# Kernel optimization log

Measured on AMD Instinct MI355X. Metric: run time of the kernel, lower is better.

Reference implementation:

```python
import jax, jax.numpy as jnp
import numpy as np

B, D, NB, H = 4096, 1024, 16, 2048
LN_EPS = 1e-5


def setup_inputs() -> dict:
    key = jax.random.key(0)
    ks = jax.random.split(key, 10)
    basis_dim = D * NB
    x = jax.random.normal(ks[0], (B, D), dtype=jnp.float32)
    ln_g = jnp.ones((D,), jnp.float32)
    ln_b = jnp.zeros((D,), jnp.float32)
    centers = jnp.tile(jnp.linspace(-2.0, 2.0, NB, dtype=jnp.float32)[None, :], (D, 1))  # [D, NB]
    width = jnp.ones((D,), jnp.float32)
    fc1_w = jax.random.normal(ks[1], (H, basis_dim), jnp.float32) / np.sqrt(basis_dim)
    fc1_b = jnp.zeros((H,), jnp.float32)
    hm_w = jax.random.normal(ks[2], (1, H), jnp.float32) / np.sqrt(H)
    hm_b = jnp.zeros((1,), jnp.float32)
    hv_w = jax.random.normal(ks[3], (1, H), jnp.float32) / np.sqrt(H)
    hv_b = jnp.zeros((1,), jnp.float32)
    sh_w = jax.random.normal(ks[4], (1, D), jnp.float32) / np.sqrt(D)
    sh_b = jnp.zeros((1,), jnp.float32)
    gamma = jnp.asarray(0.3, jnp.float32)
    return {"x": x, "ln_g": ln_g, "ln_b": ln_b, "centers": centers, "width": width,
            "fc1_w": fc1_w, "fc1_b": fc1_b, "hm_w": hm_w, "hm_b": hm_b,
            "hv_w": hv_w, "hv_b": hv_b, "sh_w": sh_w, "sh_b": sh_b, "gamma": gamma}


def reference(x, ln_g, ln_b, centers, width, fc1_w, fc1_b, hm_w, hm_b, hv_w, hv_b, sh_w, sh_b, gamma):
    # LayerNorm over in_dim
    mu = jnp.mean(x, axis=-1, keepdims=True)
    var = jnp.mean(jnp.square(x - mu), axis=-1, keepdims=True)
    x_n = (x - mu) * jax.lax.rsqrt(var + LN_EPS) * ln_g + ln_b  # [B, D]
    # triangular basis: phi[b,d,k] = relu(1 - |(x_n[b,d] - c[d,k]) / w[d]|)
    w = jax.nn.softplus(width) + 1e-6                              # [D]
    phi = jax.nn.relu(1.0 - jnp.abs((x_n[:, :, None] - centers[None]) / w[None, :, None]))
    z = phi.reshape(x.shape[0], -1)                                # [B, D*NB]
    h = jax.nn.gelu(z @ fc1_w.T + fc1_b, approximate=False)        # [B, H] (dropout = eval identity)
    y_kan_mean = h @ hm_w.T + hm_b                                 # [B, 1]
    y_lin_mean = x_n @ sh_w.T + sh_b                               # [B, 1]
    mean = y_kan_mean + jax.nn.relu(gamma) * y_lin_mean
    log_var = h @ hv_w.T + hv_b
    return (mean, log_var)
```

## Files before the change

kernel.cpp:

```cpp
#include <hip/hip_runtime.h>
#include <hip/hip_bf16.h>

#define BB 4096
#define DD 1024
#define NBF 16
#define HH 2048
#define KK 16384
#define LN_EPS 1e-5f

typedef int   i32x4 __attribute__((ext_vector_type(4)));
typedef float f32x4 __attribute__((ext_vector_type(4)));

__device__ __forceinline__ float softplusf(float x) {
  return (x > 20.f) ? x : log1pf(expf(x));
}
__device__ __forceinline__ int pack4(int q0, int q1, int q2, int q3) {
  return (q0 & 0xff) | ((q1 & 0xff) << 8) | ((q2 & 0xff) << 16) | ((q3 & 0xff) << 24);
}

__global__ void prep_kernel(const float* __restrict__ centers, const float* __restrict__ width,
                            float* __restrict__ cs) {
  const int i = blockIdx.x * 256 + threadIdx.x;
  const int d = i >> 4;
  const float w = softplusf(width[d]) + 1e-6f;
  cs[i] = centers[i] / w;
}

__global__ __launch_bounds__(256)
void zexp_kernel(const float* __restrict__ x, const float* __restrict__ g,
                 const float* __restrict__ be, const float* __restrict__ width,
                 const float* __restrict__ sh_w, const float* __restrict__ sh_b,
                 const float* __restrict__ cs,
                 unsigned char* __restrict__ zq, float* __restrict__ ylin) {
  __shared__ float red[8];
  const int b = blockIdx.x, tid = threadIdx.x;
  const float4 v = ((const float4*)(x + (size_t)b * DD))[tid];
  float s  = v.x + v.y + v.z + v.w;
  float ss = v.x*v.x + v.y*v.y + v.z*v.z + v.w*v.w;
  #pragma unroll
  for (int off = 32; off > 0; off >>= 1) {
    s  += __shfl_xor(s, off);
    ss += __shfl_xor(ss, off);
  }
  if ((tid & 63) == 0) { red[(tid>>6)*2] = s; red[(tid>>6)*2+1] = ss; }
  __syncthreads();
  const float sum   = red[0]+red[2]+red[4]+red[6];
  const float sumsq = red[1]+red[3]+red[5]+red[7];
  const float mu   = sum * (1.f/DD);
  const float var  = sumsq * (1.f/DD) - mu*mu;
  const float rstd = rsqrtf(var + LN_EPS);
  const float4 g4 = ((const float4*)g)[tid];
  const float4 b4 = ((const float4*)be)[tid];
  const float4 w4 = ((const float4*)width)[tid];
  const float4 s4 = ((const float4*)sh_w)[tid];
  const float xn0 = (v.x - mu)*rstd*g4.x + b4.x;
  const float xn1 = (v.y - mu)*rstd*g4.y + b4.y;
  const float xn2 = (v.z - mu)*rstd*g4.z + b4.z;
  const float xn3 = (v.w - mu)*rstd*g4.w + b4.w;
  float xsv[4];
  xsv[0] = xn0 / (softplusf(w4.x) + 1e-6f);
  xsv[1] = xn1 / (softplusf(w4.y) + 1e-6f);
  xsv[2] = xn2 / (softplusf(w4.z) + 1e-6f);
  xsv[3] = xn3 / (softplusf(w4.w) + 1e-6f);
  unsigned char* zr = zq + (size_t)b * KK + tid * 64;
  #pragma unroll
  for (int j = 0; j < 4; ++j) {
    const float4* c4 = (const float4*)(cs + (tid * 4 + j) * 16);
    const float xv = xsv[j];
    int q[16];
    #pragma unroll
    for (int qq = 0; qq < 4; ++qq) {
      const float4 ca = c4[qq];
      q[qq*4+0] = __float2int_rn(fmaxf(0.f, 1.f - fabsf(xv - ca.x)) * 127.f);
      q[qq*4+1] = __float2int_rn(fmaxf(0.f, 1.f - fabsf(xv - ca.y)) * 127.f);
      q[qq*4+2] = __float2int_rn(fmaxf(0.f, 1.f - fabsf(xv - ca.z)) * 127.f);
      q[qq*4+3] = __float2int_rn(fmaxf(0.f, 1.f - fabsf(xv - ca.w)) * 127.f);
    }
    int4 o;
    o.x = pack4(q[0],  q[1],  q[2],  q[3]);
    o.y = pack4(q[4],  q[5],  q[6],  q[7]);
    o.z = pack4(q[8],  q[9],  q[10], q[11]);
    o.w = pack4(q[12], q[13], q[14], q[15]);
    ((int4*)zr)[j] = o;
  }
  float yd = xn0*s4.x + xn1*s4.y + xn2*s4.z + xn3*s4.w;
  #pragma unroll
  for (int off = 32; off > 0; off >>= 1) yd += __shfl_xor(yd, off);
  __syncthreads();
  if ((tid & 63) == 0) red[tid>>6] = yd;
  __syncthreads();
  if (tid == 0) ylin[b] = red[0]+red[1]+red[2]+red[3] + sh_b[0];
}

__global__ __launch_bounds__(256)
void cvt_kernel(const float* __restrict__ w, unsigned char* __restrict__ wq,
                float* __restrict__ wscale) {
  __shared__ float red[4];
  const int j = blockIdx.x, tid = threadIdx.x;
  const float4* row4 = (const float4*)(w + (size_t)j * KK);
  float4 vv[16];
  float mx = 0.f;
  #pragma unroll
  for (int i = 0; i < 16; ++i) {
    vv[i] = row4[tid + i * 256];
    mx = fmaxf(mx, fmaxf(fmaxf(fabsf(vv[i].x), fabsf(vv[i].y)),
                         fmaxf(fabsf(vv[i].z), fabsf(vv[i].w))));
  }
  #pragma unroll
  for (int off = 32; off > 0; off >>= 1) mx = fmaxf(mx, __shfl_xor(mx, off));
  if ((tid & 63) == 0) red[tid >> 6] = mx;
  __syncthreads();
  const float smax = fmaxf(fmaxf(red[0], red[1]), fmaxf(red[2], red[3]));
  const float inv  = (smax > 0.f) ? 127.f / smax : 0.f;
  if (tid == 0) wscale[j] = smax * (1.f / 127.f);
  int* orow = (int*)(wq + (size_t)j * KK);
  #pragma unroll
  for (int i = 0; i < 16; ++i) {
    const int q0 = __float2int_rn(vv[i].x * inv);
    const int q1 = __float2int_rn(vv[i].y * inv);
    const int q2 = __float2int_rn(vv[i].z * inv);
    const int q3 = __float2int_rn(vv[i].w * inv);
    orow[tid + i * 256] = pack4(q0, q1, q2, q3);
  }
}

__global__ __launch_bounds__(256, 2)
void gemm_kernel(const unsigned char* __restrict__ zq, const unsigned char* __restrict__ wq,
                 const float* __restrict__ wscale, const float* __restrict__ fc1_b,
                 float* __restrict__ h) {
  __shared__ unsigned char As[128 * 128];
  __shared__ unsigned char Bs[128 * 128];
  const int tid  = threadIdx.x;
  const int lane = tid & 63;
  const int wv   = tid >> 6;
  const int bid = (blockIdx.x & 7) * 64 + (blockIdx.x >> 3);
  const int bm = bid & 31;
  const int bn = bid >> 5;
  const int wr = wv >> 1, wc = wv & 1;

  i32x4 acc[4][4];
  #pragma unroll
  for (int m = 0; m < 4; ++m)
    #pragma unroll
    for (int n = 0; n < 4; ++n)
      acc[m][n] = (i32x4){0, 0, 0, 0};

  const int srow   = lane >> 3;
  const int schunk = (lane & 7) ^ srow;
  const int frow = lane & 15;
  const int fkb  = lane >> 4;

  const unsigned char* zb  = zq + (size_t)(bm * 128) * KK;
  const unsigned char* wbb = wq + (size_t)(bn * 128) * KK;

  for (int t = 0; t < KK / 128; ++t) {
    const int k0 = t * 128;
    __syncthreads();
    #pragma unroll
    for (int i = 0; i < 4; ++i) {
      const int r = i * 32 + wv * 8 + srow;
      __builtin_amdgcn_global_load_lds(
          (const __attribute__((address_space(1))) void*)(zb + (size_t)r * KK + k0 + schunk * 16),
          (__attribute__((address_space(3))) void*)(&As[(i * 32 + wv * 8) * 128]), 16, 0, 0);
      __builtin_amdgcn_global_load_lds(
          (const __attribute__((address_space(1))) void*)(wbb + (size_t)r * KK + k0 + schunk * 16),
          (__attribute__((address_space(3))) void*)(&Bs[(i * 32 + wv * 8) * 128]), 16, 0, 0);
    }
    __syncthreads();
    #pragma unroll
    for (int ks = 0; ks < 2; ++ks) {
      const int kb = ks * 4 + fkb;
      i32x4 af[4], bfr[4];
      #pragma unroll
      for (int m = 0; m < 4; ++m) {
        const int Ra = wr * 64 + m * 16 + frow;
        af[m] = *reinterpret_cast<const i32x4*>(&As[Ra * 128 + ((kb ^ (Ra & 7)) * 16)]);
      }
      #pragma unroll
      for (int n = 0; n < 4; ++n) {
        const int Rb = wc * 64 + n * 16 + frow;
        bfr[n] = *reinterpret_cast<const i32x4*>(&Bs[Rb * 128 + ((kb ^ (Rb & 7)) * 16)]);
      }
      #pragma unroll
      for (int m = 0; m < 4; ++m)
        #pragma unroll
        for (int n = 0; n < 4; ++n)
          acc[m][n] = __builtin_amdgcn_mfma_i32_16x16x64_i8(af[m], bfr[n], acc[m][n], 0, 0, 0);
    }
  }
  const int row0 = bm * 128 + wr * 64;
  const int col0 = bn * 128 + wc * 64;
  #pragma unroll
  for (int n = 0; n < 4; ++n) {
    const int col = col0 + n * 16 + frow;
    const float sc   = wscale[col] * (1.f / 127.f);
    const float bias = fc1_b[col];
    #pragma unroll
    for (int m = 0; m < 4; ++m) {
      #pragma unroll
      for (int r = 0; r < 4; ++r) {
        const int row = row0 + m * 16 + fkb * 4 + r;
        const float xg = (float)acc[m][n][r] * sc + bias;
        h[(size_t)row * HH + col] = 0.5f * xg * (1.f + erff(xg * 0.70710678118f));
      }
    }
  }
}

__global__ __launch_bounds__(256)
void head_kernel(const float* __restrict__ h, const float* __restrict__ hm_w,
                 const float* __restrict__ hm_b, const float* __restrict__ hv_w,
                 const float* __restrict__ hv_b, const float* __restrict__ ylin,
                 const float* __restrict__ gamma, float* __restrict__ out) {
  __shared__ float red[8];
  const int b = blockIdx.x, tid = threadIdx.x;
  const float4* hr  = (const float4*)(h + (size_t)b * HH);
  const float4* wm  = (const float4*)hm_w;
  const float4* wvv = (const float4*)hv_w;
  float dm = 0.f, dv = 0.f;
  #pragma unroll
  for (int i = 0; i < 2; ++i) {
    const int c = tid + i * 256;
    const float4 hv4 = hr[c];
    const float4 m4  = wm[c];
    const float4 v4  = wvv[c];
    dm += hv4.x*m4.x + hv4.y*m4.y + hv4.z*m4.z + hv4.w*m4.w;
    dv += hv4.x*v4.x + hv4.y*v4.y + hv4.z*v4.z + hv4.w*v4.w;
  }
  #pragma unroll
  for (int off = 32; off > 0; off >>= 1) {
    dm += __shfl_xor(dm, off);
    dv += __shfl_xor(dv, off);
  }
  if ((tid & 63) == 0) { red[(tid>>6)*2] = dm; red[(tid>>6)*2+1] = dv; }
  __syncthreads();
  if (tid == 0) {
    const float sm = red[0]+red[2]+red[4]+red[6] + hm_b[0];
    const float sv = red[1]+red[3]+red[5]+red[7] + hv_b[0];
    out[b]      = sm + fmaxf(gamma[0], 0.f) * ylin[b];
    out[BB + b] = sv;
  }
}

extern "C" void kernel_launch(void* const* d_in, const int* in_sizes, int n_in,
                              void* d_out, int out_size, void* d_ws, size_t ws_size,
                              hipStream_t stream) {
  const float* x       = (const float*)d_in[0];
  const float* ln_g    = (const float*)d_in[1];
  const float* ln_b    = (const float*)d_in[2];
  const float* centers = (const float*)d_in[3];
  const float* width   = (const float*)d_in[4];
  const float* fc1_w   = (const float*)d_in[5];
  const float* fc1_b   = (const float*)d_in[6];
  const float* hm_w    = (const float*)d_in[7];
  const float* hm_b    = (const float*)d_in[8];
  const float* hv_w    = (const float*)d_in[9];
  const float* hv_b    = (const float*)d_in[10];
  const float* sh_w    = (const float*)d_in[11];
  const float* sh_b    = (const float*)d_in[12];
  const float* gamma   = (const float*)d_in[13];

  char* ws = (char*)d_ws;
  float* cs            = (float*)(ws);
  float* ylin          = (float*)(ws + (64 << 10));
  float* wscale        = (float*)(ws + (80 << 10));
  unsigned char* zq    = (unsigned char*)(ws + (1ull << 20));
  unsigned char* wq    = (unsigned char*)(ws + (65ull << 20));
  float* h             = (float*)(ws + (97ull << 20));
  float* out           = (float*)d_out;

  prep_kernel<<<dim3(64),   dim3(256), 0, stream>>>(centers, width, cs);
  zexp_kernel<<<dim3(4096), dim3(256), 0, stream>>>(x, ln_g, ln_b, width, sh_w, sh_b, cs, zq, ylin);
  cvt_kernel <<<dim3(2048), dim3(256), 0, stream>>>(fc1_w, wq, wscale);
  gemm_kernel<<<dim3(512),  dim3(256), 0, stream>>>(zq, wq, wscale, fc1_b, h);
  head_kernel<<<dim3(4096), dim3(256), 0, stream>>>(h, hm_w, hm_b, hv_w, hv_b, ylin, gamma, out);
}
```

Baseline: 226.6 us.

## Double-buffer int8 GEMM LDS tiles and store hidden activations as bf16

The GEMM now keeps two LDS buffers for the A and B tiles. It issues the async global-to-LDS loads for the next K tile before computing on the current one, so there is one barrier per iteration instead of two and load latency overlaps the MFMA work. The GELU output h is also stored as bf16 instead of fp32, which halves the write traffic of the GEMM epilogue and the read traffic of the head kernel. In exchange, LDS use per block doubles to 64KB, and the head dot products run on rounded bf16 activations, which may move the results slightly.

```diff
diff --git a/kernel.cpp b/kernel.cpp
--- a/kernel.cpp
+++ b/kernel.cpp
@@ -9,8 +9,17 @@
 #define LN_EPS 1e-5f
 
 typedef int   i32x4 __attribute__((ext_vector_type(4)));
-typedef float f32x4 __attribute__((ext_vector_type(4)));
-
+typedef unsigned short us8 __attribute__((ext_vector_type(8)));
+
+__device__ __forceinline__ unsigned short f2bf(float f) {
+  union { float f; unsigned int u; } c; c.f = f;
+  unsigned int u = c.u;
+  return (unsigned short)((u + 0x7FFFu + ((u >> 16) & 1u)) >> 16);
+}
+__device__ __forceinline__ float bf2f(unsigned short s) {
+  union { unsigned int u; float f; } c; c.u = ((unsigned int)s) << 16;
+  return c.f;
+}
 __device__ __forceinline__ float softplusf(float x) {
   return (x > 20.f) ? x : log1pf(expf(x));
 }
@@ -127,9 +136,9 @@
 __global__ __launch_bounds__(256, 2)
 void gemm_kernel(const unsigned char* __restrict__ zq, const unsigned char* __restrict__ wq,
                  const float* __restrict__ wscale, const float* __restrict__ fc1_b,
-                 float* __restrict__ h) {
-  __shared__ unsigned char As[128 * 128];
-  __shared__ unsigned char Bs[128 * 128];
+                 unsigned short* __restrict__ h) {
+  __shared__ unsigned char As[2][128 * 128];
+  __shared__ unsigned char Bs[2][128 * 128];
   const int tid  = threadIdx.x;
   const int lane = tid & 63;
   const int wv   = tid >> 6;
@@ -153,20 +162,27 @@
   const unsigned char* zb  = zq + (size_t)(bm * 128) * KK;
   const unsigned char* wbb = wq + (size_t)(bn * 128) * KK;
 
+  #define STAGE(buf, t) do { \
+    const int k0_ = (t) * 128; \
+    _Pragma("unroll") \
+    for (int i_ = 0; i_ < 4; ++i_) { \
+      const int r_ = i_ * 32 + wv * 8 + srow; \
+      __builtin_amdgcn_global_load_lds( \
+          (const __attribute__((address_space(1))) void*)(zb + (size_t)r_ * KK + k0_ + schunk * 16), \
+          (__attribute__((address_space(3))) void*)(&As[buf][(i_ * 32 + wv * 8) * 128]), 16, 0, 0); \
+      __builtin_amdgcn_global_load_lds( \
+          (const __attribute__((address_space(1))) void*)(wbb + (size_t)r_ * KK + k0_ + schunk * 16), \
+          (__attribute__((address_space(3))) void*)(&Bs[buf][(i_ * 32 + wv * 8) * 128]), 16, 0, 0); \
+    } \
+  } while (0)
+
+  STAGE(0, 0);
+
   for (int t = 0; t < KK / 128; ++t) {
-    const int k0 = t * 128;
     __syncthreads();
-    #pragma unroll
-    for (int i = 0; i < 4; ++i) {
-      const int r = i * 32 + wv * 8 + srow;
-      __builtin_amdgcn_global_load_lds(
-          (const __attribute__((address_space(1))) void*)(zb + (size_t)r * KK + k0 + schunk * 16),
-          (__attribute__((address_space(3))) void*)(&As[(i * 32 + wv * 8) * 128]), 16, 0, 0);
-      __builtin_amdgcn_global_load_lds(
-          (const __attribute__((address_space(1))) void*)(wbb + (size_t)r * KK + k0 + schunk * 16),
-          (__attribute__((address_space(3))) void*)(&Bs[(i * 32 + wv * 8) * 128]), 16, 0, 0);
-    }
-    __syncthreads();
+    if (t + 1 < KK / 128) STAGE((t + 1) & 1, t + 1);
+    const unsigned char* Ac = &As[t & 1][0];
+    const unsigned char* Bc = &Bs[t & 1][0];
     #pragma unroll
     for (int ks = 0; ks < 2; ++ks) {
       const int kb = ks * 4 + fkb;
@@ -174,12 +190,12 @@
       #pragma unroll
       for (int m = 0; m < 4; ++m) {
         const int Ra = wr * 64 + m * 16 + frow;
-        af[m] = *reinterpret_cast<const i32x4*>(&As[Ra * 128 + ((kb ^ (Ra & 7)) * 16)]);
+        af[m] = *reinterpret_cast<const i32x4*>(&Ac[Ra * 128 + ((kb ^ (Ra & 7)) * 16)]);
       }
       #pragma unroll
       for (int n = 0; n < 4; ++n) {
         const int Rb = wc * 64 + n * 16 + frow;
-        bfr[n] = *reinterpret_cast<const i32x4*>(&Bs[Rb * 128 + ((kb ^ (Rb & 7)) * 16)]);
+        bfr[n] = *reinterpret_cast<const i32x4*>(&Bc[Rb * 128 + ((kb ^ (Rb & 7)) * 16)]);
       }
       #pragma unroll
       for (int m = 0; m < 4; ++m)
@@ -188,6 +204,8 @@
           acc[m][n] = __builtin_amdgcn_mfma_i32_16x16x64_i8(af[m], bfr[n], acc[m][n], 0, 0, 0);
     }
   }
+  #undef STAGE
+
   const int row0 = bm * 128 + wr * 64;
   const int col0 = bn * 128 + wc * 64;
   #pragma unroll
@@ -201,32 +219,29 @@
       for (int r = 0; r < 4; ++r) {
         const int row = row0 + m * 16 + fkb * 4 + r;
         const float xg = (float)acc[m][n][r] * sc + bias;
-        h[(size_t)row * HH + col] = 0.5f * xg * (1.f + erff(xg * 0.70710678118f));
+        h[(size_t)row * HH + col] = f2bf(0.5f * xg * (1.f + erff(xg * 0.70710678118f)));
       }
     }
   }
 }
 
 __global__ __launch_bounds__(256)
-void head_kernel(const float* __restrict__ h, const float* __restrict__ hm_w,
+void head_kernel(const unsigned short* __restrict__ h, const float* __restrict__ hm_w,
                  const float* __restrict__ hm_b, const float* __restrict__ hv_w,
                  const float* __restrict__ hv_b, const float* __restrict__ ylin,
                  const float* __restrict__ gamma, float* __restrict__ out) {
   __shared__ float red[8];
   const int b = blockIdx.x, tid = threadIdx.x;
-  const float4* hr  = (const float4*)(h + (size_t)b * HH);
-  const float4* wm  = (const float4*)hm_w;
-  const float4* wvv = (const float4*)hv_w;
-  float dm = 0.f, dv = 0.f;
-  #pragma unroll
-  for (int i = 0; i < 2; ++i) {
-    const int c = tid + i * 256;
-    const float4 hv4 = hr[c];
-    const float4 m4  = wm[c];
-    const float4 v4  = wvv[c];
-    dm += hv4.x*m4.x + hv4.y*m4.y + hv4.z*m4.z + hv4.w*m4.w;
-    dv += hv4.x*v4.x + hv4.y*v4.y + hv4.z*v4.z + hv4.w*v4.w;
-  }
+  const us8 hv8 = ((const us8*)(h + (size_t)b * HH))[tid];
+  const float4 m0 = ((const float4*)hm_w)[tid*2],  m1 = ((const float4*)hm_w)[tid*2+1];
+  const float4 v0 = ((const float4*)hv_w)[tid*2],  v1 = ((const float4*)hv_w)[tid*2+1];
+  float hf[8];
+  #pragma unroll
+  for (int i = 0; i < 8; ++i) hf[i] = bf2f((unsigned short)hv8[i]);
+  float dm = hf[0]*m0.x + hf[1]*m0.y + hf[2]*m0.z + hf[3]*m0.w
+           + hf[4]*m1.x + hf[5]*m1.y + hf[6]*m1.z + hf[7]*m1.w;
+  float dv = hf[0]*v0.x + hf[1]*v0.y + hf[2]*v0.z + hf[3]*v0.w
+           + hf[4]*v1.x + hf[5]*v1.y + hf[6]*v1.z + hf[7]*v1.w;
   #pragma unroll
   for (int off = 32; off > 0; off >>= 1) {
     dm += __shfl_xor(dm, off);
@@ -266,7 +281,7 @@
   float* wscale        = (float*)(ws + (80 << 10));
   unsigned char* zq    = (unsigned char*)(ws + (1ull << 20));
   unsigned char* wq    = (unsigned char*)(ws + (65ull << 20));
-  float* h             = (float*)(ws + (97ull << 20));
+  unsigned short* h    = (unsigned short*)(ws + (97ull << 20));
   float* out           = (float*)d_out;
 
   prep_kernel<<<dim3(64),   dim3(256), 0, stream>>>(centers, width, cs);
```

After: 223.9 us. About the same (-1.2%).

## Split-K GEMM into two halves with separate merge/GELU kernel and bf16 h

Applied to the files above, without the earlier changes.

The int8 GEMM now splits the K dimension in two, launching 1024 blocks instead of 512 so more waves fill the 256 CUs, and raises the occupancy hint. Each half writes raw int32 partial sums to a workspace buffer. A new merge kernel adds the two partials and applies scale, bias and GELU, storing h as bf16, which the head kernel then reads. The cost is an extra 64 MB of int32 partial writes and reads plus one more launch, and the bf16 storage of h loses some precision.

```diff
diff --git a/kernel.cpp b/kernel.cpp
--- a/kernel.cpp
+++ b/kernel.cpp
@@ -6,11 +6,21 @@
 #define NBF 16
 #define HH 2048
 #define KK 16384
+#define NT 128
 #define LN_EPS 1e-5f
 
 typedef int   i32x4 __attribute__((ext_vector_type(4)));
-typedef float f32x4 __attribute__((ext_vector_type(4)));
-
+typedef unsigned short us8 __attribute__((ext_vector_type(8)));
+
+__device__ __forceinline__ unsigned short f2bf(float f) {
+  union { float f; unsigned int u; } c; c.f = f;
+  unsigned int u = c.u;
+  return (unsigned short)((u + 0x7FFFu + ((u >> 16) & 1u)) >> 16);
+}
+__device__ __forceinline__ float bf2f(unsigned short s) {
+  union { unsigned int u; float f; } c; c.u = ((unsigned int)s) << 16;
+  return c.f;
+}
 __device__ __forceinline__ float softplusf(float x) {
   return (x > 20.f) ? x : log1pf(expf(x));
 }
@@ -124,18 +134,19 @@
   }
 }
 
-__global__ __launch_bounds__(256, 2)
+__global__ __launch_bounds__(256, 4)
 void gemm_kernel(const unsigned char* __restrict__ zq, const unsigned char* __restrict__ wq,
-                 const float* __restrict__ wscale, const float* __restrict__ fc1_b,
-                 float* __restrict__ h) {
+                 int* __restrict__ hp) {
   __shared__ unsigned char As[128 * 128];
   __shared__ unsigned char Bs[128 * 128];
   const int tid  = threadIdx.x;
   const int lane = tid & 63;
   const int wv   = tid >> 6;
-  const int bid = (blockIdx.x & 7) * 64 + (blockIdx.x >> 3);
-  const int bm = bid & 31;
-  const int bn = bid >> 5;
+  const int bid  = (blockIdx.x & 7) * 128 + (blockIdx.x >> 3);
+  const int tile = bid & 511;
+  const int kh   = bid >> 9;
+  const int bm = tile & 31;
+  const int bn = tile >> 5;
   const int wr = wv >> 1, wc = wv & 1;
 
   i32x4 acc[4][4];
@@ -153,7 +164,8 @@
   const unsigned char* zb  = zq + (size_t)(bm * 128) * KK;
   const unsigned char* wbb = wq + (size_t)(bn * 128) * KK;
 
-  for (int t = 0; t < KK / 128; ++t) {
+  const int t0 = kh * 64, t1 = t0 + 64;
+  for (int t = t0; t < t1; ++t) {
     const int k0 = t * 128;
     __syncthreads();
     #pragma unroll
@@ -188,45 +200,65 @@
           acc[m][n] = __builtin_amdgcn_mfma_i32_16x16x64_i8(af[m], bfr[n], acc[m][n], 0, 0, 0);
     }
   }
+
+  int* hpo = hp + (size_t)kh * BB * HH;
   const int row0 = bm * 128 + wr * 64;
   const int col0 = bn * 128 + wc * 64;
   #pragma unroll
   for (int n = 0; n < 4; ++n) {
     const int col = col0 + n * 16 + frow;
-    const float sc   = wscale[col] * (1.f / 127.f);
-    const float bias = fc1_b[col];
     #pragma unroll
     for (int m = 0; m < 4; ++m) {
       #pragma unroll
       for (int r = 0; r < 4; ++r) {
         const int row = row0 + m * 16 + fkb * 4 + r;
-        const float xg = (float)acc[m][n][r] * sc + bias;
-        h[(size_t)row * HH + col] = 0.5f * xg * (1.f + erff(xg * 0.70710678118f));
+        hpo[(size_t)row * HH + col] = acc[m][n][r];
       }
     }
   }
 }
 
 __global__ __launch_bounds__(256)
-void head_kernel(const float* __restrict__ h, const float* __restrict__ hm_w,
+void merge_kernel(const int* __restrict__ hp, const float* __restrict__ wscale,
+                  const float* __restrict__ fc1_b, unsigned short* __restrict__ h) {
+  const int row = blockIdx.x, tid = threadIdx.x;
+  const int c0 = tid * 8;
+  const int4 a0 = *(const int4*)&hp[(size_t)row * HH + c0];
+  const int4 a1 = *(const int4*)&hp[(size_t)row * HH + c0 + 4];
+  const int4 b0 = *(const int4*)&hp[(size_t)BB * HH + (size_t)row * HH + c0];
+  const int4 b1 = *(const int4*)&hp[(size_t)BB * HH + (size_t)row * HH + c0 + 4];
+  const float4 s0 = ((const float4*)wscale)[tid*2], s1 = ((const float4*)wscale)[tid*2+1];
+  const float4 f0 = ((const float4*)fc1_b)[tid*2],  f1 = ((const float4*)fc1_b)[tid*2+1];
+  int   sums[8] = {a0.x+b0.x, a0.y+b0.y, a0.z+b0.z, a0.w+b0.w,
+                   a1.x+b1.x, a1.y+b1.y, a1.z+b1.z, a1.w+b1.w};
+  float scs[8]  = {s0.x, s0.y, s0.z, s0.w, s1.x, s1.y, s1.z, s1.w};
+  float bis[8]  = {f0.x, f0.y, f0.z, f0.w, f1.x, f1.y, f1.z, f1.w};
+  us8 o;
+  #pragma unroll
+  for (int j = 0; j < 8; ++j) {
+    const float xg = (float)sums[j] * (scs[j] * (1.f / 127.f)) + bis[j];
+    o[j] = f2bf(0.5f * xg * (1.f + erff(xg * 0.70710678118f)));
+  }
+  *(us8*)&h[(size_t)row * HH + c0] = o;
+}
+
+__global__ __launch_bounds__(256)
+void head_kernel(const unsigned short* __restrict__ h, const float* __restrict__ hm_w,
                  const float* __restrict__ hm_b, const float* __restrict__ hv_w,
                  const float* __restrict__ hv_b, const float* __restrict__ ylin,
                  const float* __restrict__ gamma, float* __restrict__ out) {
   __shared__ float red[8];
   const int b = blockIdx.x, tid = threadIdx.x;
-  const float4* hr  = (const float4*)(h + (size_t)b * HH);
-  const float4* wm  = (const float4*)hm_w;
-  const float4* wvv = (const float4*)hv_w;
-  float dm = 0.f, dv = 0.f;
-  #pragma unroll
-  for (int i = 0; i < 2; ++i) {
-    const int c = tid + i * 256;
-    const float4 hv4 = hr[c];
-    const float4 m4  = wm[c];
-    const float4 v4  = wvv[c];
-    dm += hv4.x*m4.x + hv4.y*m4.y + hv4.z*m4.z + hv4.w*m4.w;
-    dv += hv4.x*v4.x + hv4.y*v4.y + hv4.z*v4.z + hv4.w*v4.w;
-  }
+  const us8 hv8 = ((const us8*)(h + (size_t)b * HH))[tid];
+  const float4 m0 = ((const float4*)hm_w)[tid*2],  m1 = ((const float4*)hm_w)[tid*2+1];
+  const float4 v0 = ((const float4*)hv_w)[tid*2],  v1 = ((const float4*)hv_w)[tid*2+1];
+  float hf[8];
+  #pragma unroll
+  for (int i = 0; i < 8; ++i) hf[i] = bf2f((unsigned short)hv8[i]);
+  float dm = hf[0]*m0.x + hf[1]*m0.y + hf[2]*m0.z + hf[3]*m0.w
+           + hf[4]*m1.x + hf[5]*m1.y + hf[6]*m1.z + hf[7]*m1.w;
+  float dv = hf[0]*v0.x + hf[1]*v0.y + hf[2]*v0.z + hf[3]*v0.w
+           + hf[4]*v1.x + hf[5]*v1.y + hf[6]*v1.z + hf[7]*v1.w;
   #pragma unroll
   for (int off = 32; off > 0; off >>= 1) {
     dm += __shfl_xor(dm, off);
@@ -266,12 +298,14 @@
   float* wscale        = (float*)(ws + (80 << 10));
   unsigned char* zq    = (unsigned char*)(ws + (1ull << 20));
   unsigned char* wq    = (unsigned char*)(ws + (65ull << 20));
-  float* h             = (float*)(ws + (97ull << 20));
+  int* hp              = (int*)(ws + (97ull << 20));
+  unsigned short* h    = (unsigned short*)(ws + (161ull << 20));
   float* out           = (float*)d_out;
 
-  prep_kernel<<<dim3(64),   dim3(256), 0, stream>>>(centers, width, cs);
-  zexp_kernel<<<dim3(4096), dim3(256), 0, stream>>>(x, ln_g, ln_b, width, sh_w, sh_b, cs, zq, ylin);
-  cvt_kernel <<<dim3(2048), dim3(256), 0, stream>>>(fc1_w, wq, wscale);
-  gemm_kernel<<<dim3(512),  dim3(256), 0, stream>>>(zq, wq, wscale, fc1_b, h);
-  head_kernel<<<dim3(4096), dim3(256), 0, stream>>>(h, hm_w, hm_b, hv_w, hv_b, ylin, gamma, out);
-}
+  prep_kernel <<<dim3(64),   dim3(256), 0, stream>>>(centers, width, cs);
+  zexp_kernel <<<dim3(4096), dim3(256), 0, stream>>>(x, ln_g, ln_b, width, sh_w, sh_b, cs, zq, ylin);
+  cvt_kernel  <<<dim3(2048), dim3(256), 0, stream>>>(fc1_w, wq, wscale);
+  gemm_kernel <<<dim3(1024), dim3(256), 0, stream>>>(zq, wq, hp);
+  merge_kernel<<<dim3(4096), dim3(256), 0, stream>>>(hp, wscale, fc1_b, h);
+  head_kernel <<<dim3(4096), dim3(256), 0, stream>>>(h, hm_w, hm_b, hv_w, hv_b, ylin, gamma, out);
+}
```

Result: slower. 245.3 us (+8.3%).
